# Performance work log

Hardware: AMD Instinct MI355X
Metric: run time of the kernel (lower is better)

## Reference

```python
import jax, jax.numpy as jnp
import numpy as np

THRESHOLD = 1.0
SCHMITT_TEMP = 0.1
N_FIRES = 128  # target_fires; torch computes N dynamically, fixed here for jit
LN_EPS = 1e-5


def setup_inputs() -> dict:
    key = jax.random.key(0)
    ks = jax.random.split(key, 12)
    B, T, C = 16, 3000, 32
    H, W, Dsw = 32, 375, 192
    P, dp, dm, hid = 32, 32, 512, 128  # polyphony, pitch_token_dim, d_model, cif_hidden_dim
    f32 = jnp.float32
    return {
        "fire_signal": jax.random.normal(ks[0], (B, T, C), f32),
        "swin_2d": jax.random.normal(ks[1], (B, H, W, Dsw), f32),
        "pitch_tokens": jax.random.normal(ks[2], (B, N_FIRES, P, dp), f32),
        "target_lengths": jax.random.randint(ks[3], (B,), 1, N_FIRES),
        # learned parameters
        "conv_w": jax.random.normal(ks[4], (C, 1, 3), f32) * 0.3,   # depthwise conv1d, groups=C, no bias
        "ln_w": jnp.ones((C,), f32),
        "ln_b": jnp.zeros((C,), f32),
        "dense_w": jax.random.normal(ks[5], (C, hid), f32) * 0.18,
        "dense_b": jnp.zeros((hid,), f32),
        "proj_w": jax.random.normal(ks[6], (hid, 1), f32) * 0.09,
        "proj_b": jnp.zeros((1,), f32),
        "pitch_w": jax.random.normal(ks[7], (dp, dm), f32) * 0.18,
        "pitch_b": jnp.zeros((dm,), f32),
        "swin_w": jax.random.normal(ks[8], (Dsw, dm), f32) * 0.07,
        "swin_b": jnp.zeros((dm,), f32),
    }


def _compute_alpha(fire_signal, conv_w, ln_w, ln_b, dense_w, dense_b, proj_w, proj_b):
    # depthwise conv over time + residual, then LN -> Linear -> ReLU -> Linear -> Softplus
    ctx = fire_signal.transpose(0, 2, 1)  # [B,C,T]
    C = ctx.shape[1]
    mem = jax.lax.conv_general_dilated(
        ctx, conv_w, window_strides=(1,), padding='SAME',
        feature_group_count=C, dimension_numbers=('NCH', 'OIH', 'NCH'))
    x = (mem + ctx).transpose(0, 2, 1)  # [B,T,C]
    mu = jnp.mean(x, axis=-1, keepdims=True)
    var = jnp.var(x, axis=-1, keepdims=True)
    x = (x - mu) * jax.lax.rsqrt(var + LN_EPS) * ln_w + ln_b
    x = jax.nn.relu(x @ dense_w + dense_b)
    alpha = jax.nn.softplus(x @ proj_w + proj_b)[..., 0]  # [B,T]
    return alpha


def reference(fire_signal, swin_2d, pitch_tokens, target_lengths,
              conv_w, ln_w, ln_b, dense_w, dense_b, proj_w, proj_b,
              pitch_w, pitch_b, swin_w, swin_b):
    B, T, _ = fire_signal.shape
    H, W = swin_2d.shape[1], swin_2d.shape[2]

    # --- compute_fires ---
    alpha = _compute_alpha(fire_signal, conv_w, ln_w, ln_b,
                           dense_w, dense_b, proj_w, proj_b)
    onset_prob = jax.nn.sigmoid((alpha - THRESHOLD) / SCHMITT_TEMP)
    qty_loss = jnp.mean(jnp.abs(onset_prob.sum(axis=1) - target_lengths.astype(alpha.dtype)))
    fire_cumsum = jnp.cumsum((alpha > THRESHOLD).astype(jnp.int32), axis=1)  # [B,T]
    slot_targets = jnp.arange(1, N_FIRES + 1, dtype=jnp.int32)  # [N]
    fire_frames = jax.vmap(lambda c: jnp.searchsorted(c, slot_targets))(fire_cumsum)
    fire_frames = jnp.minimum(fire_frames, T - 1)  # [B,N]

    # --- forward: assemble acoustic token sequences ---
    fire_w = jnp.clip((fire_frames.astype(jnp.float32) * W / T).astype(jnp.int32), 0, W - 1)
    # gather swin freq slices at fire time positions: [B,H,N,Dsw]
    swin_at = jnp.take_along_axis(swin_2d, fire_w[:, None, :, None], axis=2)
    swin_at = swin_at.transpose(0, 2, 1, 3)  # [B,N,H,Dsw]
    swin_tok = swin_at @ swin_w + swin_b      # [B,N,H,d_model]
    pitch_tok = pitch_tokens @ pitch_w + pitch_b  # [B,N,P,d_model]
    acoustic = jnp.concatenate([pitch_tok, swin_tok], axis=2)  # [B,N,P+H,d_model]
    return acoustic, alpha, qty_loss
```

## Files before the change

### kernel.cpp

```cpp
#include <hip/hip_runtime.h>
#include <math.h>

#define T_FIRE 3000
#define B_SZ 16
#define C_CH 32
#define HID 128
#define NF 128
#define H_SW 32
#define W_SW 375
#define DSW 192
#define DM 512
#define P_POLY 32
#define DP 32

typedef __attribute__((ext_vector_type(8))) short bf16x8;
typedef __attribute__((ext_vector_type(4))) float f32x4;

__device__ inline short f2bf(float f) {
    union { float f; unsigned u; } v; v.f = f;
    unsigned r = v.u + 0x7FFF + ((v.u >> 16) & 1);
    return (short)(r >> 16);
}

__device__ inline bf16x8 load_afrag(const float* __restrict__ p) {
    float4 x = *(const float4*)p;
    float4 y = *(const float4*)(p + 4);
    bf16x8 f;
    f[0] = f2bf(x.x); f[1] = f2bf(x.y); f[2] = f2bf(x.z); f[3] = f2bf(x.w);
    f[4] = f2bf(y.x); f[5] = f2bf(y.y); f[6] = f2bf(y.z); f[7] = f2bf(y.w);
    return f;
}

__global__ __launch_bounds__(256) void alpha_kernel(
    const float* __restrict__ fs, const float* __restrict__ conv_w,
    const float* __restrict__ ln_w, const float* __restrict__ ln_b,
    const float* __restrict__ dense_w, const float* __restrict__ dense_b,
    const float* __restrict__ proj_w, const float* __restrict__ proj_b,
    float* __restrict__ alpha_out)
{
    int lane = threadIdx.x & 63;
    int wave = threadIdx.x >> 6;
    int r = blockIdx.x * 4 + wave;
    int b = r / T_FIRE, t = r - b * T_FIRE;
    int c = lane & 31;
    long base = ((long)(b * T_FIRE + t)) * C_CH + c;
    float xc = fs[base];
    float xm = (t > 0)          ? fs[base - C_CH] : 0.f;
    float xp = (t < T_FIRE - 1) ? fs[base + C_CH] : 0.f;
    float w0 = conv_w[c * 3 + 0], w1 = conv_w[c * 3 + 1], w2 = conv_w[c * 3 + 2];
    float x = xc + xm * w0 + xc * w1 + xp * w2;
    float s = x, s2 = x * x;
#pragma unroll
    for (int o = 1; o < 64; o <<= 1) { s += __shfl_xor(s, o); s2 += __shfl_xor(s2, o); }
    float mean = s * (1.f / 64.f);
    float var  = s2 * (1.f / 64.f) - mean * mean;
    float xn = (x - mean) * rsqrtf(var + 1e-5f) * ln_w[c] + ln_b[c];
    float a0 = dense_b[lane], a1 = dense_b[lane + 64];
#pragma unroll
    for (int cc = 0; cc < 32; cc++) {
        float xv = __shfl(xn, cc);
        a0 = fmaf(xv, dense_w[cc * HID + lane], a0);
        a1 = fmaf(xv, dense_w[cc * HID + lane + 64], a1);
    }
    a0 = fmaxf(a0, 0.f);
    a1 = fmaxf(a1, 0.f);
    float v = a0 * proj_w[lane] + a1 * proj_w[lane + 64];
#pragma unroll
    for (int o = 1; o < 64; o <<= 1) v += __shfl_xor(v, o);
    if (lane == 0) {
        float z = v + proj_b[0];
        alpha_out[r] = fmaxf(z, 0.f) + log1pf(expf(-fabsf(z)));
    }
}

__global__ __launch_bounds__(1024) void fires_kernel(
    const float* __restrict__ alpha, const int* __restrict__ target,
    int* __restrict__ fw, float* __restrict__ qpart)
{
    __shared__ int wtot[16];
    __shared__ int sbase;
    __shared__ float ssig[16];
    int b = blockIdx.x, tid = threadIdx.x;
    int lane = tid & 63, w = tid >> 6;
    if (tid < NF) fw[b * NF + tid] = (T_FIRE - 1) >> 3;
    if (tid == 0) sbase = 0;
    float psig = 0.f;
    __syncthreads();
    for (int chunk = 0; chunk < 3; chunk++) {
        int idx = chunk * 1024 + tid;
        bool valid = idx < T_FIRE;
        float a = valid ? alpha[b * T_FIRE + idx] : 0.f;
        if (valid) psig += 1.f / (1.f + expf(-(a - 1.0f) * 10.f));
        bool flag = valid && (a > 1.0f);
        unsigned long long mask = __ballot(flag);
        int prefix = __popcll(mask & ((1ull << lane) - 1ull));
        if (lane == 0) wtot[w] = __popcll(mask);
        __syncthreads();
        if (tid == 0) {
            int run = sbase;
            for (int i = 0; i < 16; i++) { int v2 = wtot[i]; wtot[i] = run; run += v2; }
            sbase = run;
        }
        __syncthreads();
        int rank = wtot[w] + prefix;
        if (flag && rank < NF) fw[b * NF + rank] = idx >> 3;
        __syncthreads();
    }
#pragma unroll
    for (int o = 1; o < 64; o <<= 1) psig += __shfl_xor(psig, o);
    if (lane == 0) ssig[w] = psig;
    __syncthreads();
    if (tid == 0) {
        float tot = 0.f;
        for (int i = 0; i < 16; i++) tot += ssig[i];
        qpart[b] = fabsf(tot - (float)target[b]);
    }
}

__global__ void qty_kernel(const float* __restrict__ qpart, float* __restrict__ out)
{
    int lane = threadIdx.x;
    float v = (lane < B_SZ) ? qpart[lane] : 0.f;
#pragma unroll
    for (int o = 1; o < 64; o <<= 1) v += __shfl_xor(v, o);
    if (lane == 0) out[0] = v * (1.f / B_SZ);
}

__global__ __launch_bounds__(256) void pack_kernel(
    const float* __restrict__ pw, const float* __restrict__ sww,
    short* __restrict__ bp_p, short* __restrict__ bp_s)
{
    int t = blockIdx.x * 256 + threadIdx.x;
    if (t < 12288) {
        int lane = t & 63;
        int ct = (t >> 6) & 31;
        int ks = t >> 11;
        int k0 = ks * 32 + (lane >> 4) * 8;
        int n  = ct * 16 + (lane & 15);
        bf16x8 v;
#pragma unroll
        for (int j = 0; j < 8; j++) v[j] = f2bf(sww[(k0 + j) * DM + n]);
        *(bf16x8*)(bp_s + (long)t * 8) = v;
    } else if (t < 14336) {
        int u = t - 12288;
        int lane = u & 63;
        int ct = u >> 6;
        int k0 = (lane >> 4) * 8;
        int n  = ct * 16 + (lane & 15);
        bf16x8 v;
#pragma unroll
        for (int j = 0; j < 8; j++) v[j] = f2bf(pw[(k0 + j) * DM + n]);
        *(bf16x8*)(bp_p + (long)u * 8) = v;
    }
}

__global__ __launch_bounds__(512) void tok_kernel(
    const float* __restrict__ pt, const float* __restrict__ sw2d,
    const short* __restrict__ bp_p, const short* __restrict__ bp_s,
    const float* __restrict__ pb, const float* __restrict__ swb,
    const int* __restrict__ fw, float* __restrict__ acoustic)
{
    int bn = blockIdx.x;
    int b  = bn >> 7;
    int w    = threadIdx.x >> 6;
    int lane = threadIdx.x & 63;
    int quad = lane >> 4, m16 = lane & 15;
    int sec  = w >> 2;
    int band = (w >> 1) & 1;
    int ch   = w & 1;

    f32x4 acc[16];
#pragma unroll
    for (int i = 0; i < 16; i++) acc[i] = (f32x4){0.f, 0.f, 0.f, 0.f};

    if (sec == 0) {
        const float* arow = pt + ((long)bn * 32 + band * 16 + m16) * DP + quad * 8;
        bf16x8 af = load_afrag(arow);
        const bf16x8* bpp = (const bf16x8*)bp_p;
#pragma unroll
        for (int ct = 0; ct < 16; ct++) {
            bf16x8 bf_ = bpp[(long)(ch * 16 + ct) * 64 + lane];
            acc[ct] = __builtin_amdgcn_mfma_f32_16x16x32_bf16(af, bf_, acc[ct], 0, 0, 0);
        }
    } else {
        int wcol = fw[bn];
        const float* arow =
            sw2d + (((long)(b * H_SW + band * 16 + m16)) * W_SW + wcol) * DSW + quad * 8;
        const bf16x8* bps = (const bf16x8*)bp_s;
#pragma unroll 1
        for (int ks = 0; ks < 6; ks++) {
            bf16x8 af = load_afrag(arow + ks * 32);
#pragma unroll
            for (int ct = 0; ct < 16; ct++) {
                bf16x8 bf_ = bps[(long)(ks * 32 + ch * 16 + ct) * 64 + lane];
                acc[ct] = __builtin_amdgcn_mfma_f32_16x16x32_bf16(af, bf_, acc[ct], 0, 0, 0);
            }
        }
    }

    const float* bias = (sec == 0) ? pb : swb;
    long rowbase = ((long)bn * 64 + sec * 32 + band * 16 + quad * 4) * DM;
#pragma unroll
    for (int ct = 0; ct < 16; ct++) {
        int col = ch * 256 + ct * 16 + m16;
        float bv = bias[col];
#pragma unroll
        for (int r = 0; r < 4; r++)
            acoustic[rowbase + (long)r * DM + col] = acc[ct][r] + bv;
    }
}

extern "C" void kernel_launch(void* const* d_in, const int* in_sizes, int n_in,
                              void* d_out, int out_size, void* d_ws, size_t ws_size,
                              hipStream_t stream)
{
    const float* fs      = (const float*)d_in[0];
    const float* swin2d  = (const float*)d_in[1];
    const float* pt      = (const float*)d_in[2];
    const int*   target  = (const int*)d_in[3];
    const float* conv_w  = (const float*)d_in[4];
    const float* ln_w    = (const float*)d_in[5];
    const float* ln_b    = (const float*)d_in[6];
    const float* dense_w = (const float*)d_in[7];
    const float* dense_b = (const float*)d_in[8];
    const float* proj_w  = (const float*)d_in[9];
    const float* proj_b  = (const float*)d_in[10];
    const float* pitch_w = (const float*)d_in[11];
    const float* pitch_b = (const float*)d_in[12];
    const float* swin_w  = (const float*)d_in[13];
    const float* swin_b  = (const float*)d_in[14];

    float* out      = (float*)d_out;
    float* acoustic = out;
    float* alpha    = out + (long)B_SZ * NF * 64 * DM;
    float* qty      = alpha + B_SZ * T_FIRE;

    char* ws = (char*)d_ws;
    int*   fw    = (int*)ws;                                  ws += B_SZ * NF * sizeof(int);
    float* qpart = (float*)ws;                                ws += 64 * sizeof(float);
    short* bp_s  = (short*)ws;                                ws += (long)DSW * DM * sizeof(short);
    short* bp_p  = (short*)ws;                                ws += (long)DP * DM * sizeof(short);

    alpha_kernel<<<B_SZ * T_FIRE / 4, 256, 0, stream>>>(
        fs, conv_w, ln_w, ln_b, dense_w, dense_b, proj_w, proj_b, alpha);
    pack_kernel<<<56, 256, 0, stream>>>(pitch_w, swin_w, bp_p, bp_s);
    fires_kernel<<<B_SZ, 1024, 0, stream>>>(alpha, target, fw, qpart);
    qty_kernel<<<1, 64, 0, stream>>>(qpart, qty);
    tok_kernel<<<B_SZ * NF, 512, 0, stream>>>(
        pt, swin2d, bp_p, bp_s, pitch_b, swin_b, fw, acoustic);
}
```

Baseline: 466.6 us.

## Fuse pack into alpha kernel, fold qty reduction into tok, hoist A loads, use nontemporal stores

Merges the weight-packing kernel into the alpha kernel as extra blocks, and moves the final qty mean into the first block of the token kernel, cutting two launches. In the token kernel, all six swin A-fragments are now loaded up front so the MFMA loop no longer waits on a global load each k-step. Output stores to the large acoustic tensor become nontemporal to avoid cache pollution. The cost is more registers for the preloaded fragments and slightly uneven block work.

```diff
diff --git a/kernel.cpp b/kernel.cpp
--- a/kernel.cpp
+++ b/kernel.cpp
@@ -13,6 +13,8 @@
 #define P_POLY 32
 #define DP 32
 
+#define ALPHA_BLOCKS (B_SZ * T_FIRE / 4)
+
 typedef __attribute__((ext_vector_type(8))) short bf16x8;
 typedef __attribute__((ext_vector_type(4))) float f32x4;
 
@@ -31,13 +33,41 @@
     return f;
 }
 
-__global__ __launch_bounds__(256) void alpha_kernel(
+__global__ __launch_bounds__(256) void alpha_pack_kernel(
     const float* __restrict__ fs, const float* __restrict__ conv_w,
     const float* __restrict__ ln_w, const float* __restrict__ ln_b,
     const float* __restrict__ dense_w, const float* __restrict__ dense_b,
     const float* __restrict__ proj_w, const float* __restrict__ proj_b,
-    float* __restrict__ alpha_out)
-{
+    float* __restrict__ alpha_out,
+    const float* __restrict__ pw, const float* __restrict__ sww,
+    short* __restrict__ bp_p, short* __restrict__ bp_s)
+{
+    if (blockIdx.x >= ALPHA_BLOCKS) {
+        int t = (blockIdx.x - ALPHA_BLOCKS) * 256 + threadIdx.x;
+        if (t < 12288) {
+            int lane = t & 63;
+            int ct = (t >> 6) & 31;
+            int ks = t >> 11;
+            int k0 = ks * 32 + (lane >> 4) * 8;
+            int n  = ct * 16 + (lane & 15);
+            bf16x8 v;
+#pragma unroll
+            for (int j = 0; j < 8; j++) v[j] = f2bf(sww[(k0 + j) * DM + n]);
+            *(bf16x8*)(bp_s + (long)t * 8) = v;
+        } else if (t < 14336) {
+            int u = t - 12288;
+            int lane = u & 63;
+            int ct = u >> 6;
+            int k0 = (lane >> 4) * 8;
+            int n  = ct * 16 + (lane & 15);
+            bf16x8 v;
+#pragma unroll
+            for (int j = 0; j < 8; j++) v[j] = f2bf(pw[(k0 + j) * DM + n]);
+            *(bf16x8*)(bp_p + (long)u * 8) = v;
+        }
+        return;
+    }
+
     int lane = threadIdx.x & 63;
     int wave = threadIdx.x >> 6;
     int r = blockIdx.x * 4 + wave;
@@ -117,48 +147,12 @@
     }
 }
 
-__global__ void qty_kernel(const float* __restrict__ qpart, float* __restrict__ out)
-{
-    int lane = threadIdx.x;
-    float v = (lane < B_SZ) ? qpart[lane] : 0.f;
-#pragma unroll
-    for (int o = 1; o < 64; o <<= 1) v += __shfl_xor(v, o);
-    if (lane == 0) out[0] = v * (1.f / B_SZ);
-}
-
-__global__ __launch_bounds__(256) void pack_kernel(
-    const float* __restrict__ pw, const float* __restrict__ sww,
-    short* __restrict__ bp_p, short* __restrict__ bp_s)
-{
-    int t = blockIdx.x * 256 + threadIdx.x;
-    if (t < 12288) {
-        int lane = t & 63;
-        int ct = (t >> 6) & 31;
-        int ks = t >> 11;
-        int k0 = ks * 32 + (lane >> 4) * 8;
-        int n  = ct * 16 + (lane & 15);
-        bf16x8 v;
-#pragma unroll
-        for (int j = 0; j < 8; j++) v[j] = f2bf(sww[(k0 + j) * DM + n]);
-        *(bf16x8*)(bp_s + (long)t * 8) = v;
-    } else if (t < 14336) {
-        int u = t - 12288;
-        int lane = u & 63;
-        int ct = u >> 6;
-        int k0 = (lane >> 4) * 8;
-        int n  = ct * 16 + (lane & 15);
-        bf16x8 v;
-#pragma unroll
-        for (int j = 0; j < 8; j++) v[j] = f2bf(pw[(k0 + j) * DM + n]);
-        *(bf16x8*)(bp_p + (long)u * 8) = v;
-    }
-}
-
 __global__ __launch_bounds__(512) void tok_kernel(
     const float* __restrict__ pt, const float* __restrict__ sw2d,
     const short* __restrict__ bp_p, const short* __restrict__ bp_s,
     const float* __restrict__ pb, const float* __restrict__ swb,
-    const int* __restrict__ fw, float* __restrict__ acoustic)
+    const int* __restrict__ fw, float* __restrict__ acoustic,
+    const float* __restrict__ qpart, float* __restrict__ qty_out)
 {
     int bn = blockIdx.x;
     int b  = bn >> 7;
@@ -169,6 +163,12 @@
     int band = (w >> 1) & 1;
     int ch   = w & 1;
 
+    if (bn == 0 && threadIdx.x == 0) {
+        float tot = 0.f;
+        for (int i = 0; i < B_SZ; i++) tot += qpart[i];
+        qty_out[0] = tot * (1.f / B_SZ);
+    }
+
     f32x4 acc[16];
 #pragma unroll
     for (int i = 0; i < 16; i++) acc[i] = (f32x4){0.f, 0.f, 0.f, 0.f};
@@ -186,14 +186,16 @@
         int wcol = fw[bn];
         const float* arow =
             sw2d + (((long)(b * H_SW + band * 16 + m16)) * W_SW + wcol) * DSW + quad * 8;
+        bf16x8 af[6];
+#pragma unroll
+        for (int ks = 0; ks < 6; ks++) af[ks] = load_afrag(arow + ks * 32);
         const bf16x8* bps = (const bf16x8*)bp_s;
 #pragma unroll 1
         for (int ks = 0; ks < 6; ks++) {
-            bf16x8 af = load_afrag(arow + ks * 32);
 #pragma unroll
             for (int ct = 0; ct < 16; ct++) {
                 bf16x8 bf_ = bps[(long)(ks * 32 + ch * 16 + ct) * 64 + lane];
-                acc[ct] = __builtin_amdgcn_mfma_f32_16x16x32_bf16(af, bf_, acc[ct], 0, 0, 0);
+                acc[ct] = __builtin_amdgcn_mfma_f32_16x16x32_bf16(af[ks], bf_, acc[ct], 0, 0, 0);
             }
         }
     }
@@ -206,7 +208,8 @@
         float bv = bias[col];
 #pragma unroll
         for (int r = 0; r < 4; r++)
-            acoustic[rowbase + (long)r * DM + col] = acc[ct][r] + bv;
+            __builtin_nontemporal_store(acc[ct][r] + bv,
+                                        &acoustic[rowbase + (long)r * DM + col]);
     }
 }
 
@@ -241,11 +244,10 @@
     short* bp_s  = (short*)ws;                                ws += (long)DSW * DM * sizeof(short);
     short* bp_p  = (short*)ws;                                ws += (long)DP * DM * sizeof(short);
 
-    alpha_kernel<<<B_SZ * T_FIRE / 4, 256, 0, stream>>>(
-        fs, conv_w, ln_w, ln_b, dense_w, dense_b, proj_w, proj_b, alpha);
-    pack_kernel<<<56, 256, 0, stream>>>(pitch_w, swin_w, bp_p, bp_s);
+    alpha_pack_kernel<<<ALPHA_BLOCKS + 56, 256, 0, stream>>>(
+        fs, conv_w, ln_w, ln_b, dense_w, dense_b, proj_w, proj_b, alpha,
+        pitch_w, swin_w, bp_p, bp_s);
     fires_kernel<<<B_SZ, 1024, 0, stream>>>(alpha, target, fw, qpart);
-    qty_kernel<<<1, 64, 0, stream>>>(qpart, qty);
     tok_kernel<<<B_SZ * NF, 512, 0, stream>>>(
-        pt, swin2d, bp_p, bp_s, pitch_b, swin_b, fw, acoustic);
-}
+        pt, swin2d, bp_p, bp_s, pitch_b, swin_b, fw, acoustic, qpart, qty);
+}
```

After: 512.3 us. +9.8%, slower.
